# Kernel tuning notes

Hardware: AMD Instinct MI355X
Metric: run time of the kernel (lower is better)

Reference implementation:

```python
import jax, jax.numpy as jnp
import numpy as np

# Static configuration matching the selected code path:
#   mode='inject_subject', is_self_attn=True, layer_id='up_blocks.0' (inject layer, bank hit)
#   alpha = AlphaScheduler.alpha(step=20, total=50, 'up_blocks.0') = 0.8 * 0.6 = 0.48
B, L, D, H = 4, 1024, 1280, 20
DH = D // H  # 64
ALPHA = 0.48


def setup_inputs() -> dict:
    key = jax.random.key(0)
    ks = jax.random.split(key, 8)
    w = lambda k, shp: (jax.random.normal(k, shp, dtype=jnp.float32) * 0.02)
    return {
        "hidden_states": jax.random.normal(ks[0], (B, L, D), dtype=jnp.float32),
        "Wq": w(ks[1], (D, D)),
        "Wk": w(ks[2], (D, D)),
        "Wv": w(ks[3], (D, D)),
        "Wo": w(ks[4], (D, D)),
        "bo": jnp.zeros((D,), dtype=jnp.float32),
        # cached background K/V, stored after head_to_batch_dim -> [B*H, L_bg, DH]
        "K_bg": jax.random.normal(ks[5], (B * H, L, DH), dtype=jnp.float32),
        "V_bg": jax.random.normal(ks[6], (B * H, L, DH), dtype=jnp.float32),
    }


def _head_to_batch(x):  # [B, L, D] -> [B*H, L, DH]
    b, l, _ = x.shape
    return x.reshape(b, l, H, DH).transpose(0, 2, 1, 3).reshape(b * H, l, DH)


def _batch_to_head(x):  # [B*H, L, DH] -> [B, L, D]
    bh, l, _ = x.shape
    b = bh // H
    return x.reshape(b, H, l, DH).transpose(0, 2, 1, 3).reshape(b, l, D)


def reference(hidden_states, Wq, Wk, Wv, Wo, bo, K_bg, V_bg):
    # q/k/v projections (self-attention: k, v from hidden_states)
    q = _head_to_batch(hidden_states @ Wq)  # [B*H, L, DH]
    k = _head_to_batch(hidden_states @ Wk)
    v = _head_to_batch(hidden_states @ Wv)

    # inject_subject: concat cached background K/V scaled by alpha along kv-seq dim
    k = jnp.concatenate([k, ALPHA * K_bg], axis=1)  # [B*H, 2L, DH]
    v = jnp.concatenate([v, ALPHA * V_bg], axis=1)

    # _sdpa: q scaled by scale*sqrt(dh), SDPA divides by sqrt(dh) -> net factor `scale`
    scale = 1.0 / jnp.sqrt(jnp.asarray(DH, dtype=q.dtype))
    scores = jnp.einsum('bqd,bkd->bqk', q, k) * scale  # [B*H, L, 2L]
    probs = jax.nn.softmax(scores, axis=-1)
    context = jnp.einsum('bqk,bkd->bqd', probs, v)  # [B*H, L, DH]

    out = _batch_to_head(context) @ Wo + bo  # to_out[0] linear
    return out
```

## Files before the change

kernel.cpp:

```cpp
#include <hip/hip_runtime.h>
#include <hip/hip_bf16.h>

#define B_   4
#define L_   1024
#define D_   1280
#define H_   20
#define DH_  64
#define BH_  (B_*H_)
#define L2_  (2*L_)
#define ALPHA_ 0.48f
#define QSCALE_ 0.180336880f

typedef __attribute__((ext_vector_type(8))) short short8;
typedef __attribute__((ext_vector_type(4))) float float4v;

#define EXP2(x) exp2f(x)

__device__ __forceinline__ float bf2f(ushort u) {
    union { unsigned int i; float f; } v; v.i = ((unsigned int)u) << 16; return v.f;
}
__device__ __forceinline__ ushort f2bf(float f) {
    union { float f; unsigned int i; } v; v.f = f;
    unsigned int i = v.i;
    unsigned int r = i + 0x7FFF + ((i >> 16) & 1);
    return (ushort)(r >> 16);
}
__device__ __forceinline__ short8 pack8(float4 f0, float4 f1) {
    short8 o;
    o[0] = (short)f2bf(f0.x); o[1] = (short)f2bf(f0.y);
    o[2] = (short)f2bf(f0.z); o[3] = (short)f2bf(f0.w);
    o[4] = (short)f2bf(f1.x); o[5] = (short)f2bf(f1.y);
    o[6] = (short)f2bf(f1.z); o[7] = (short)f2bf(f1.w);
    return o;
}
__device__ __forceinline__ void pack4_store(ushort* dst, float a, float b, float c, float d) {
    union { __hip_bfloat162 h; unsigned int u; } x, y;
    x.h = __float22bfloat162_rn(make_float2(a, b));
    y.h = __float22bfloat162_rn(make_float2(c, d));
    uint2 v; v.x = x.u; v.y = y.u;
    *(uint2*)dst = v;
}

__device__ __forceinline__ void async16(const void* g, void* l) {
    __builtin_amdgcn_global_load_lds(
        (__attribute__((address_space(1))) void*)g,
        (__attribute__((address_space(3))) void*)l, 16, 0, 0);
}

__global__ __launch_bounds__(256) void detect_dtype(const unsigned int* __restrict__ w,
                                                    int* __restrict__ flag) {
    __shared__ int cnt;
    if (threadIdx.x == 0) cnt = 0;
    __syncthreads();
    int local = 0;
    for (int i = threadIdx.x; i < 4096; i += 256) {
        unsigned e = (w[i] >> 7) & 0xFF;
        local += (e >= 100 && e <= 130) ? 1 : 0;
    }
    atomicAdd(&cnt, local);
    __syncthreads();
    if (threadIdx.x == 0) flag[0] = (cnt > 2048) ? 1 : 0;
}

__global__ __launch_bounds__(256) void prep(
    const void* __restrict__ w0, const void* __restrict__ w1,
    const void* __restrict__ w2, const void* __restrict__ w3,
    ushort* __restrict__ Wt,
    const void* __restrict__ Vbg, ushort* __restrict__ Vt,
    const void* __restrict__ X, ushort* __restrict__ Xb,
    const void* __restrict__ Kbg, ushort* __restrict__ Kcv,
    const int* __restrict__ flag) {
    bool is16 = flag[0] != 0;
    int bi = blockIdx.x, tid = threadIdx.x;
    if (bi < 2880) {
        bool doScale = (bi >= 1600);
        const void* src; ushort* dst; int srcld, dstld; long sbase, dbase;
        if (bi < 1600) {
            int z = bi / 400, t4 = bi % 400;
            int by = t4 / 20, bx = t4 % 20;
            const void* srcs[4] = {w0, w1, w2, w3};
            src = srcs[z]; srcld = D_; dstld = D_;
            sbase = (long)(by * 64) * D_ + bx * 64;
            dst = Wt + (long)z * D_ * D_;
            dbase = (long)(bx * 64) * D_ + by * 64;
        } else {
            int j = bi - 1600;
            int bh = j >> 4, kt = j & 15;
            src = Vbg; srcld = DH_; dstld = L2_;
            sbase = ((long)bh * L_ + kt * 64) * DH_;
            dst = Vt;
            dbase = (long)bh * DH_ * L2_ + L_ + kt * 64;
        }
        __shared__ ushort t[64 * 72];
        int ldr = tid >> 3, ldc = (tid & 7) * 8;
#pragma unroll
        for (int i = 0; i < 2; i++) {
            int y = ldr + 32 * i;
            long idx = sbase + (long)y * srcld + ldc;
            short8 v;
            if (is16) {
                v = *(const short8*)((const ushort*)src + idx);
                if (doScale) {
#pragma unroll
                    for (int j2 = 0; j2 < 8; j2++)
                        v[j2] = (short)f2bf(ALPHA_ * bf2f((ushort)v[j2]));
                }
            } else {
                const float* s = (const float*)src;
                float4 f0 = *(const float4*)&s[idx];
                float4 f1 = *(const float4*)&s[idx + 4];
                if (doScale) {
                    f0.x *= ALPHA_; f0.y *= ALPHA_; f0.z *= ALPHA_; f0.w *= ALPHA_;
                    f1.x *= ALPHA_; f1.y *= ALPHA_; f1.z *= ALPHA_; f1.w *= ALPHA_;
                }
                v = pack8(f0, f1);
            }
            *(short8*)&t[y * 72 + ldc] = v;
        }
        __syncthreads();
        int c = tid & 63, r0 = (tid >> 6) * 16;
#pragma unroll
        for (int i = 0; i < 2; i++) {
            short8 o;
#pragma unroll
            for (int j2 = 0; j2 < 8; j2++) o[j2] = (short)t[(r0 + i * 8 + j2) * 72 + c];
            *(short8*)&dst[dbase + (long)c * dstld + r0 + i * 8] = o;
        }
    } else if (bi < 5440) {
        if (is16) return;
        long i = ((long)(bi - 2880) * 256 + tid) * 8;
        const float* s = (const float*)X;
        *(short8*)&Xb[i] = pack8(*(const float4*)&s[i], *(const float4*)&s[i + 4]);
    } else {
        if (is16) return;
        long i = ((long)(bi - 5440) * 256 + tid) * 8;
        const float* s = (const float*)Kbg;
        *(short8*)&Kcv[i] = pack8(*(const float4*)&s[i], *(const float4*)&s[i + 4]);
    }
}

template<int BMt, int BNt, int WROWS, int WCOLS>
__global__ __launch_bounds__(256) void gemm_tpl(
    const ushort* __restrict__ A16, const void* __restrict__ Araw,
    const ushort* __restrict__ Bt,
    ushort* __restrict__ Qp, ushort* __restrict__ Kp, ushort* __restrict__ Vt,
    void* __restrict__ Out, const void* __restrict__ bo, int mode,
    const int* __restrict__ flag) {
    constexpr int MI = BMt / WROWS / 16;
    constexpr int NI = BNt / WCOLS / 16;
    constexpr int ASZ = BMt * 32, BSZ = BNt * 32;
    constexpr int RB = 1280 / BNt;
    __shared__ __align__(16) ushort Al[2 * ASZ];
    __shared__ __align__(16) ushort Bl[2 * BSZ];
    bool is16 = flag[0] != 0;
    const ushort* A = (mode == 0 && is16) ? (const ushort*)Araw : A16;
    int tid = threadIdx.x;
    int bx = blockIdx.x, by = blockIdx.y;
    int w = tid >> 6, lane = tid & 63, l15 = lane & 15, quad = lane >> 4;
    int wm = (w / WCOLS) * (BMt / WROWS);
    int wn = (w % WCOLS) * (BNt / WCOLS);
    float4v acc[MI][NI] = {};
    const int K = 1280;
    constexpr int NK = 40;
    const ushort* Arow = A + (long)by * BMt * K + (tid >> 2) * K + (tid & 3) * 8;
    const ushort* Brow = Bt + (long)bx * BNt * K + (tid >> 2) * K + (tid & 3) * 8;

    auto stage = [&](int ki, int b) {
#pragma unroll
        for (int i = 0; i < BMt / 64; i++)
            async16(Arow + (long)i * 64 * K + ki * 32, &Al[b * ASZ + (i * 4 + w) * 512]);
#pragma unroll
        for (int i = 0; i < BNt / 64; i++)
            async16(Brow + (long)i * 64 * K + ki * 32, &Bl[b * BSZ + (i * 4 + w) * 512]);
    };

    stage(0, 0);
    __syncthreads();
    for (int ki = 0; ki < NK; ki++) {
        int cur = ki & 1;
        if (ki + 1 < NK) stage(ki + 1, 1 - cur);
        short8 av[MI], bv[NI];
#pragma unroll
        for (int mi = 0; mi < MI; mi++)
            av[mi] = *(const short8*)&Al[cur * ASZ + (wm + mi * 16 + l15) * 32 + quad * 8];
#pragma unroll
        for (int ni = 0; ni < NI; ni++)
            bv[ni] = *(const short8*)&Bl[cur * BSZ + (wn + ni * 16 + l15) * 32 + quad * 8];
#pragma unroll
        for (int mi = 0; mi < MI; mi++)
#pragma unroll
            for (int ni = 0; ni < NI; ni++)
                acc[mi][ni] = __builtin_amdgcn_mfma_f32_16x16x32_bf16(av[mi], bv[ni], acc[mi][ni], 0, 0, 0);
        __syncthreads();
    }

    if (mode == 0) {
        int which = bx / RB;
#pragma unroll
        for (int mi = 0; mi < MI; mi++) {
            int m0 = by * BMt + wm + mi * 16 + quad * 4;
            int b = m0 >> 10, l0 = m0 & 1023;
#pragma unroll
            for (int ni = 0; ni < NI; ni++) {
                int n = bx * BNt + wn + ni * 16 + l15;
                int np = n - which * 1280;
                int h = np >> 6, dh = np & 63;
                if (which == 0) {
#pragma unroll
                    for (int r = 0; r < 4; r++)
                        Qp[((long)(b * H_ + h) * L_ + l0 + r) * DH_ + dh] =
                            f2bf(acc[mi][ni][r] * QSCALE_);
                } else if (which == 1) {
#pragma unroll
                    for (int r = 0; r < 4; r++)
                        Kp[((long)(b * H_ + h) * L_ + l0 + r) * DH_ + dh] =
                            f2bf(acc[mi][ni][r]);
                } else {
                    pack4_store(&Vt[((long)(b * H_ + h) * DH_ + dh) * L2_ + l0],
                                acc[mi][ni][0], acc[mi][ni][1],
                                acc[mi][ni][2], acc[mi][ni][3]);
                }
            }
        }
    } else {
#pragma unroll
        for (int mi = 0; mi < MI; mi++) {
            int mloc = wm + mi * 16 + quad * 4;
#pragma unroll
            for (int ni = 0; ni < NI; ni++) {
                int nloc = wn + ni * 16 + l15;
#pragma unroll
                for (int r = 0; r < 4; r++) {
                    int m = by * BMt + mloc + r;
                    int n = bx * BNt + nloc;
                    float bias = is16 ? bf2f(((const ushort*)bo)[n]) : ((const float*)bo)[n];
                    float o = acc[mi][ni][r] + bias;
                    if (is16) ((ushort*)Out)[(long)m * D_ + n] = f2bf(o);
                    else      ((float*)Out)[(long)m * D_ + n] = o;
                }
            }
        }
    }
}

#define FS 72

__global__ __launch_bounds__(256) void flash_attn(
    const ushort* __restrict__ Qp, const ushort* __restrict__ Kp,
    const void* __restrict__ KbgRaw, const ushort* __restrict__ Kcv,
    const ushort* __restrict__ Vt, ushort* __restrict__ Ctx,
    const int* __restrict__ flag) {
    __shared__ __align__(16) ushort Kl[2 * 4096], Vl[2 * 4096];
    __shared__ __align__(16) ushort Pl[128 * FS];
    const ushort* Kbg = flag[0] ? (const ushort*)KbgRaw : Kcv;
    int tid = threadIdx.x;
    int w = tid >> 6, lane = tid & 63, l15 = lane & 15, quad = lane >> 4;
    int bi = blockIdx.x;
    int bh = (bi & 7) * 10 + ((bi >> 3) % 10);
    int qt = bi / 80;

    short8 aq[2][2];
    const ushort* Qb = Qp + ((long)bh * L_ + qt * 128 + w * 32) * DH_;
#pragma unroll
    for (int mi = 0; mi < 2; mi++)
#pragma unroll
        for (int ks = 0; ks < 2; ks++)
            aq[mi][ks] = *(const short8*)&Qb[(mi * 16 + l15) * DH_ + ks * 32 + quad * 8];

    float rs[2] = {0.f, 0.f};
    float4v O[2][4] = {};
    const ushort* Vb = Vt + (long)bh * DH_ * L2_;
    int prow = (w * 32 + l15) * FS;

    auto stage = [&](int kt, int b) {
        const ushort* Ksrc = (kt < 16)
            ? Kp  + ((long)bh * L_ + kt * 64) * DH_
            : Kbg + ((long)bh * L_ + (kt - 16) * 64) * DH_;
#pragma unroll
        for (int i = 0; i < 2; i++) {
            int q = i * 4 + w;
            async16(&Ksrc[(long)lane * DH_ + q * 8], &Kl[b * 4096 + q * 512]);
            async16(&Vb[(long)lane * L2_ + kt * 64 + q * 8], &Vl[b * 4096 + q * 512]);
        }
    };

    stage(0, 0);
    __syncthreads();
    for (int kt = 0; kt < 32; kt++) {
        int cur = kt & 1;
        if (kt + 1 < 32) stage(kt + 1, 1 - cur);
        bool bg = (kt >= 16);
        short8 bk[2][4];
#pragma unroll
        for (int ks = 0; ks < 2; ks++)
#pragma unroll
            for (int nt = 0; nt < 4; nt++)
                bk[ks][nt] = *(const short8*)&Kl[cur * 4096 + (ks * 4 + quad) * 512 + (nt * 16 + l15) * 8];
#pragma unroll
        for (int mi = 0; mi < 2; mi++) {
            float4v s[4] = {};
#pragma unroll
            for (int ks = 0; ks < 2; ks++)
#pragma unroll
                for (int nt = 0; nt < 4; nt++)
                    s[nt] = __builtin_amdgcn_mfma_f32_16x16x32_bf16(bk[ks][nt], aq[mi][ks], s[nt], 0, 0, 0);
#pragma unroll
            for (int nt = 0; nt < 4; nt++) {
                float p[4];
#pragma unroll
                for (int r = 0; r < 4; r++) {
                    float sv = s[nt][r];
                    if (bg) sv *= ALPHA_;
                    p[r] = EXP2(sv);
                    rs[mi] += p[r];
                }
                pack4_store(&Pl[prow + mi * 16 * FS + nt * 16 + quad * 4],
                            p[0], p[1], p[2], p[3]);
            }
        }
        short8 bv[2][4];
#pragma unroll
        for (int ks = 0; ks < 2; ks++)
#pragma unroll
            for (int nt = 0; nt < 4; nt++)
                bv[ks][nt] = *(const short8*)&Vl[cur * 4096 + (ks * 4 + quad) * 512 + (nt * 16 + l15) * 8];
        asm volatile("s_waitcnt lgkmcnt(0)" ::: "memory");
#pragma unroll
        for (int mi = 0; mi < 2; mi++)
#pragma unroll
            for (int ks = 0; ks < 2; ks++) {
                short8 ap = *(const short8*)&Pl[prow + mi * 16 * FS + ks * 32 + quad * 8];
#pragma unroll
                for (int nt = 0; nt < 4; nt++)
                    O[mi][nt] = __builtin_amdgcn_mfma_f32_16x16x32_bf16(bv[ks][nt], ap, O[mi][nt], 0, 0, 0);
            }
        __syncthreads();
    }
    float rcp[2];
#pragma unroll
    for (int mi = 0; mi < 2; mi++) {
        float v = rs[mi];
        v += __shfl_xor(v, 16);
        v += __shfl_xor(v, 32);
        rcp[mi] = 1.f / v;
    }
    int b = bh / H_, h = bh % H_;
#pragma unroll
    for (int mi = 0; mi < 2; mi++) {
        long l = qt * 128 + w * 32 + mi * 16 + l15;
#pragma unroll
        for (int nt = 0; nt < 4; nt++)
            pack4_store(&Ctx[(long)(b * L_ + l) * D_ + h * DH_ + nt * 16 + quad * 4],
                        O[mi][nt][0] * rcp[mi], O[mi][nt][1] * rcp[mi],
                        O[mi][nt][2] * rcp[mi], O[mi][nt][3] * rcp[mi]);
    }
}

extern "C" void kernel_launch(void* const* d_in, const int* in_sizes, int n_in,
                              void* d_out, int out_size, void* d_ws, size_t ws_size,
                              hipStream_t stream) {
    const void* X   = d_in[0];
    const void* Wq  = d_in[1];
    const void* Wk  = d_in[2];
    const void* Wv  = d_in[3];
    const void* Wo  = d_in[4];
    const void* bo  = d_in[5];
    const void* Kbg = d_in[6];
    const void* Vbg = d_in[7];

    char* ws = (char*)d_ws;
    size_t off = 0;
    auto alloc = [&](size_t bytes) {
        void* p = ws + off;
        off = (off + bytes + 255) & ~(size_t)255;
        return p;
    };
    int*    dflag = (int*)alloc(256);
    ushort* Wt    = (ushort*)alloc((size_t)4 * D_ * D_ * 2);
    ushort* Qp    = (ushort*)alloc((size_t)BH_ * L_ * DH_ * 2);
    ushort* Kp    = (ushort*)alloc((size_t)BH_ * L_ * DH_ * 2);
    ushort* Kcv   = (ushort*)alloc((size_t)BH_ * L_ * DH_ * 2);
    ushort* Vt    = (ushort*)alloc((size_t)BH_ * DH_ * L2_ * 2);
    ushort* Xb    = (ushort*)alloc((size_t)B_ * L_ * D_ * 2);
    ushort* Ctx   = Xb;
    ushort* Wqkv_t = Wt;
    ushort* Wo_t   = Wt + (size_t)3 * D_ * D_;

    dim3 tb(256);
    detect_dtype<<<1, tb, 0, stream>>>((const unsigned int*)Wq, dflag);
    prep<<<8000, tb, 0, stream>>>(Wq, Wk, Wv, Wo, Wt, Vbg, Vt, X, Xb, Kbg, Kcv, dflag);
    gemm_tpl<128, 64, 2, 2><<<dim3(60, 32), tb, 0, stream>>>(
        Xb, X, Wqkv_t, Qp, Kp, Vt, nullptr, nullptr, 0, dflag);
    flash_attn<<<dim3(640), tb, 0, stream>>>(Qp, Kp, Kbg, Kcv, Vt, Ctx, dflag);
    gemm_tpl<64, 64, 2, 2><<<dim3(20, 64), tb, 0, stream>>>(
        Ctx, nullptr, Wo_t, nullptr, nullptr, nullptr, d_out, bo, 1, dflag);
}
```

Before: 349.2 us.

## Software-pipeline PV MFMA one tile behind QK in flash attention, drop dtype detection

In the flash-attention loop, the P·V MFMA for the previous key tile now runs after the current tile's QK^T MFMAs. K and V staging is split so V for a tile is loaded one iteration later than K. This is meant to hide the exp/LDS-store latency and save one barrier per iteration. The change also swaps exp2f for a raw v_exp_f32 and removes the runtime dtype-detection kernel and its fp32/bf16 branches, so the code now assumes fp32 inputs.

```diff
diff --git a/kernel.cpp b/kernel.cpp
--- a/kernel.cpp
+++ b/kernel.cpp
@@ -14,11 +14,12 @@
 typedef __attribute__((ext_vector_type(8))) short short8;
 typedef __attribute__((ext_vector_type(4))) float float4v;
 
-#define EXP2(x) exp2f(x)
-
-__device__ __forceinline__ float bf2f(ushort u) {
-    union { unsigned int i; float f; } v; v.i = ((unsigned int)u) << 16; return v.f;
-}
+__device__ __forceinline__ float exp2_fast(float x) {
+    float r;
+    asm volatile("v_exp_f32 %0, %1" : "=v"(r) : "v"(x));
+    return r;
+}
+
 __device__ __forceinline__ ushort f2bf(float f) {
     union { float f; unsigned int i; } v; v.f = f;
     unsigned int i = v.i;
@@ -47,38 +48,21 @@
         (__attribute__((address_space(3))) void*)l, 16, 0, 0);
 }
 
-__global__ __launch_bounds__(256) void detect_dtype(const unsigned int* __restrict__ w,
-                                                    int* __restrict__ flag) {
-    __shared__ int cnt;
-    if (threadIdx.x == 0) cnt = 0;
-    __syncthreads();
-    int local = 0;
-    for (int i = threadIdx.x; i < 4096; i += 256) {
-        unsigned e = (w[i] >> 7) & 0xFF;
-        local += (e >= 100 && e <= 130) ? 1 : 0;
-    }
-    atomicAdd(&cnt, local);
-    __syncthreads();
-    if (threadIdx.x == 0) flag[0] = (cnt > 2048) ? 1 : 0;
-}
-
 __global__ __launch_bounds__(256) void prep(
-    const void* __restrict__ w0, const void* __restrict__ w1,
-    const void* __restrict__ w2, const void* __restrict__ w3,
+    const float* __restrict__ w0, const float* __restrict__ w1,
+    const float* __restrict__ w2, const float* __restrict__ w3,
     ushort* __restrict__ Wt,
-    const void* __restrict__ Vbg, ushort* __restrict__ Vt,
-    const void* __restrict__ X, ushort* __restrict__ Xb,
-    const void* __restrict__ Kbg, ushort* __restrict__ Kcv,
-    const int* __restrict__ flag) {
-    bool is16 = flag[0] != 0;
+    const float* __restrict__ Vbg, ushort* __restrict__ Vt,
+    const float* __restrict__ X, ushort* __restrict__ Xb,
+    const float* __restrict__ Kbg, ushort* __restrict__ Kcv) {
     int bi = blockIdx.x, tid = threadIdx.x;
     if (bi < 2880) {
         bool doScale = (bi >= 1600);
-        const void* src; ushort* dst; int srcld, dstld; long sbase, dbase;
+        const float* src; ushort* dst; int srcld, dstld; long sbase, dbase;
         if (bi < 1600) {
             int z = bi / 400, t4 = bi % 400;
             int by = t4 / 20, bx = t4 % 20;
-            const void* srcs[4] = {w0, w1, w2, w3};
+            const float* srcs[4] = {w0, w1, w2, w3};
             src = srcs[z]; srcld = D_; dstld = D_;
             sbase = (long)(by * 64) * D_ + bx * 64;
             dst = Wt + (long)z * D_ * D_;
@@ -97,25 +81,13 @@
         for (int i = 0; i < 2; i++) {
             int y = ldr + 32 * i;
             long idx = sbase + (long)y * srcld + ldc;
-            short8 v;
-            if (is16) {
-                v = *(const short8*)((const ushort*)src + idx);
-                if (doScale) {
-#pragma unroll
-                    for (int j2 = 0; j2 < 8; j2++)
-                        v[j2] = (short)f2bf(ALPHA_ * bf2f((ushort)v[j2]));
-                }
-            } else {
-                const float* s = (const float*)src;
-                float4 f0 = *(const float4*)&s[idx];
-                float4 f1 = *(const float4*)&s[idx + 4];
-                if (doScale) {
-                    f0.x *= ALPHA_; f0.y *= ALPHA_; f0.z *= ALPHA_; f0.w *= ALPHA_;
-                    f1.x *= ALPHA_; f1.y *= ALPHA_; f1.z *= ALPHA_; f1.w *= ALPHA_;
-                }
-                v = pack8(f0, f1);
-            }
-            *(short8*)&t[y * 72 + ldc] = v;
+            float4 f0 = *(const float4*)&src[idx];
+            float4 f1 = *(const float4*)&src[idx + 4];
+            if (doScale) {
+                f0.x *= ALPHA_; f0.y *= ALPHA_; f0.z *= ALPHA_; f0.w *= ALPHA_;
+                f1.x *= ALPHA_; f1.y *= ALPHA_; f1.z *= ALPHA_; f1.w *= ALPHA_;
+            }
+            *(short8*)&t[y * 72 + ldc] = pack8(f0, f1);
         }
         __syncthreads();
         int c = tid & 63, r0 = (tid >> 6) * 16;
@@ -127,33 +99,25 @@
             *(short8*)&dst[dbase + (long)c * dstld + r0 + i * 8] = o;
         }
     } else if (bi < 5440) {
-        if (is16) return;
         long i = ((long)(bi - 2880) * 256 + tid) * 8;
-        const float* s = (const float*)X;
-        *(short8*)&Xb[i] = pack8(*(const float4*)&s[i], *(const float4*)&s[i + 4]);
+        *(short8*)&Xb[i] = pack8(*(const float4*)&X[i], *(const float4*)&X[i + 4]);
     } else {
-        if (is16) return;
         long i = ((long)(bi - 5440) * 256 + tid) * 8;
-        const float* s = (const float*)Kbg;
-        *(short8*)&Kcv[i] = pack8(*(const float4*)&s[i], *(const float4*)&s[i + 4]);
+        *(short8*)&Kcv[i] = pack8(*(const float4*)&Kbg[i], *(const float4*)&Kbg[i + 4]);
     }
 }
 
 template<int BMt, int BNt, int WROWS, int WCOLS>
 __global__ __launch_bounds__(256) void gemm_tpl(
-    const ushort* __restrict__ A16, const void* __restrict__ Araw,
-    const ushort* __restrict__ Bt,
+    const ushort* __restrict__ A, const ushort* __restrict__ Bt,
     ushort* __restrict__ Qp, ushort* __restrict__ Kp, ushort* __restrict__ Vt,
-    void* __restrict__ Out, const void* __restrict__ bo, int mode,
-    const int* __restrict__ flag) {
+    float* __restrict__ Out, const float* __restrict__ bo, int mode) {
     constexpr int MI = BMt / WROWS / 16;
     constexpr int NI = BNt / WCOLS / 16;
     constexpr int ASZ = BMt * 32, BSZ = BNt * 32;
     constexpr int RB = 1280 / BNt;
     __shared__ __align__(16) ushort Al[2 * ASZ];
     __shared__ __align__(16) ushort Bl[2 * BSZ];
-    bool is16 = flag[0] != 0;
-    const ushort* A = (mode == 0 && is16) ? (const ushort*)Araw : A16;
     int tid = threadIdx.x;
     int bx = blockIdx.x, by = blockIdx.y;
     int w = tid >> 6, lane = tid & 63, l15 = lane & 15, quad = lane >> 4;
@@ -233,10 +197,7 @@
                 for (int r = 0; r < 4; r++) {
                     int m = by * BMt + mloc + r;
                     int n = bx * BNt + nloc;
-                    float bias = is16 ? bf2f(((const ushort*)bo)[n]) : ((const float*)bo)[n];
-                    float o = acc[mi][ni][r] + bias;
-                    if (is16) ((ushort*)Out)[(long)m * D_ + n] = f2bf(o);
-                    else      ((float*)Out)[(long)m * D_ + n] = o;
+                    Out[(long)m * D_ + n] = acc[mi][ni][r] + bo[n];
                 }
             }
         }
@@ -247,12 +208,10 @@
 
 __global__ __launch_bounds__(256) void flash_attn(
     const ushort* __restrict__ Qp, const ushort* __restrict__ Kp,
-    const void* __restrict__ KbgRaw, const ushort* __restrict__ Kcv,
-    const ushort* __restrict__ Vt, ushort* __restrict__ Ctx,
-    const int* __restrict__ flag) {
+    const ushort* __restrict__ Kbg, const ushort* __restrict__ Vt,
+    ushort* __restrict__ Ctx) {
     __shared__ __align__(16) ushort Kl[2 * 4096], Vl[2 * 4096];
     __shared__ __align__(16) ushort Pl[128 * FS];
-    const ushort* Kbg = flag[0] ? (const ushort*)KbgRaw : Kcv;
     int tid = threadIdx.x;
     int w = tid >> 6, lane = tid & 63, l15 = lane & 15, quad = lane >> 4;
     int bi = blockIdx.x;
@@ -272,58 +231,86 @@
     const ushort* Vb = Vt + (long)bh * DH_ * L2_;
     int prow = (w * 32 + l15) * FS;
 
-    auto stage = [&](int kt, int b) {
+    auto stageK = [&](int kt) {
         const ushort* Ksrc = (kt < 16)
             ? Kp  + ((long)bh * L_ + kt * 64) * DH_
             : Kbg + ((long)bh * L_ + (kt - 16) * 64) * DH_;
 #pragma unroll
         for (int i = 0; i < 2; i++) {
             int q = i * 4 + w;
-            async16(&Ksrc[(long)lane * DH_ + q * 8], &Kl[b * 4096 + q * 512]);
-            async16(&Vb[(long)lane * L2_ + kt * 64 + q * 8], &Vl[b * 4096 + q * 512]);
+            async16(&Ksrc[(long)lane * DH_ + q * 8], &Kl[(kt & 1) * 4096 + q * 512]);
         }
     };
-
-    stage(0, 0);
+    auto stageV = [&](int kt) {
+#pragma unroll
+        for (int i = 0; i < 2; i++) {
+            int q = i * 4 + w;
+            async16(&Vb[(long)lane * L2_ + kt * 64 + q * 8], &Vl[(kt & 1) * 4096 + q * 512]);
+        }
+    };
+
+    stageK(0);
     __syncthreads();
     for (int kt = 0; kt < 32; kt++) {
         int cur = kt & 1;
-        if (kt + 1 < 32) stage(kt + 1, 1 - cur);
-        bool bg = (kt >= 16);
+        if (kt + 1 < 32) stageK(kt + 1);
+        stageV(kt);
         short8 bk[2][4];
 #pragma unroll
         for (int ks = 0; ks < 2; ks++)
 #pragma unroll
             for (int nt = 0; nt < 4; nt++)
                 bk[ks][nt] = *(const short8*)&Kl[cur * 4096 + (ks * 4 + quad) * 512 + (nt * 16 + l15) * 8];
-#pragma unroll
-        for (int mi = 0; mi < 2; mi++) {
-            float4v s[4] = {};
+        float4v s[2][4] = {};
+#pragma unroll
+        for (int mi = 0; mi < 2; mi++)
 #pragma unroll
             for (int ks = 0; ks < 2; ks++)
 #pragma unroll
                 for (int nt = 0; nt < 4; nt++)
-                    s[nt] = __builtin_amdgcn_mfma_f32_16x16x32_bf16(bk[ks][nt], aq[mi][ks], s[nt], 0, 0, 0);
+                    s[mi][nt] = __builtin_amdgcn_mfma_f32_16x16x32_bf16(bk[ks][nt], aq[mi][ks], s[mi][nt], 0, 0, 0);
+        if (kt > 0) {
+            short8 bv[2][4];
+#pragma unroll
+            for (int ks = 0; ks < 2; ks++)
+#pragma unroll
+                for (int nt = 0; nt < 4; nt++)
+                    bv[ks][nt] = *(const short8*)&Vl[(1 - cur) * 4096 + (ks * 4 + quad) * 512 + (nt * 16 + l15) * 8];
+#pragma unroll
+            for (int mi = 0; mi < 2; mi++)
+#pragma unroll
+                for (int ks = 0; ks < 2; ks++) {
+                    short8 ap = *(const short8*)&Pl[prow + mi * 16 * FS + ks * 32 + quad * 8];
+#pragma unroll
+                    for (int nt = 0; nt < 4; nt++)
+                        O[mi][nt] = __builtin_amdgcn_mfma_f32_16x16x32_bf16(bv[ks][nt], ap, O[mi][nt], 0, 0, 0);
+                }
+        }
+        bool bg = (kt >= 16);
+#pragma unroll
+        for (int mi = 0; mi < 2; mi++)
 #pragma unroll
             for (int nt = 0; nt < 4; nt++) {
                 float p[4];
 #pragma unroll
                 for (int r = 0; r < 4; r++) {
-                    float sv = s[nt][r];
+                    float sv = s[mi][nt][r];
                     if (bg) sv *= ALPHA_;
-                    p[r] = EXP2(sv);
+                    p[r] = exp2_fast(sv);
                     rs[mi] += p[r];
                 }
                 pack4_store(&Pl[prow + mi * 16 * FS + nt * 16 + quad * 4],
                             p[0], p[1], p[2], p[3]);
             }
-        }
+        __syncthreads();
+    }
+    {
         short8 bv[2][4];
 #pragma unroll
         for (int ks = 0; ks < 2; ks++)
 #pragma unroll
             for (int nt = 0; nt < 4; nt++)
-                bv[ks][nt] = *(const short8*)&Vl[cur * 4096 + (ks * 4 + quad) * 512 + (nt * 16 + l15) * 8];
+                bv[ks][nt] = *(const short8*)&Vl[4096 + (ks * 4 + quad) * 512 + (nt * 16 + l15) * 8];
         asm volatile("s_waitcnt lgkmcnt(0)" ::: "memory");
 #pragma unroll
         for (int mi = 0; mi < 2; mi++)
@@ -334,7 +321,6 @@
                 for (int nt = 0; nt < 4; nt++)
                     O[mi][nt] = __builtin_amdgcn_mfma_f32_16x16x32_bf16(bv[ks][nt], ap, O[mi][nt], 0, 0, 0);
             }
-        __syncthreads();
     }
     float rcp[2];
 #pragma unroll
@@ -359,14 +345,14 @@
 extern "C" void kernel_launch(void* const* d_in, const int* in_sizes, int n_in,
                               void* d_out, int out_size, void* d_ws, size_t ws_size,
                               hipStream_t stream) {
-    const void* X   = d_in[0];
-    const void* Wq  = d_in[1];
-    const void* Wk  = d_in[2];
-    const void* Wv  = d_in[3];
-    const void* Wo  = d_in[4];
-    const void* bo  = d_in[5];
-    const void* Kbg = d_in[6];
-    const void* Vbg = d_in[7];
+    const float* X   = (const float*)d_in[0];
+    const float* Wq  = (const float*)d_in[1];
+    const float* Wk  = (const float*)d_in[2];
+    const float* Wv  = (const float*)d_in[3];
+    const float* Wo  = (const float*)d_in[4];
+    const float* bo  = (const float*)d_in[5];
+    const float* Kbg = (const float*)d_in[6];
+    const float* Vbg = (const float*)d_in[7];
 
     char* ws = (char*)d_ws;
     size_t off = 0;
@@ -375,7 +361,6 @@
         off = (off + bytes + 255) & ~(size_t)255;
         return p;
     };
-    int*    dflag = (int*)alloc(256);
     ushort* Wt    = (ushort*)alloc((size_t)4 * D_ * D_ * 2);
     ushort* Qp    = (ushort*)alloc((size_t)BH_ * L_ * DH_ * 2);
     ushort* Kp    = (ushort*)alloc((size_t)BH_ * L_ * DH_ * 2);
@@ -387,11 +372,10 @@
     ushort* Wo_t   = Wt + (size_t)3 * D_ * D_;
 
     dim3 tb(256);
-    detect_dtype<<<1, tb, 0, stream>>>((const unsigned int*)Wq, dflag);
-    prep<<<8000, tb, 0, stream>>>(Wq, Wk, Wv, Wo, Wt, Vbg, Vt, X, Xb, Kbg, Kcv, dflag);
+    prep<<<8000, tb, 0, stream>>>(Wq, Wk, Wv, Wo, Wt, Vbg, Vt, X, Xb, Kbg, Kcv);
     gemm_tpl<128, 64, 2, 2><<<dim3(60, 32), tb, 0, stream>>>(
-        Xb, X, Wqkv_t, Qp, Kp, Vt, nullptr, nullptr, 0, dflag);
-    flash_attn<<<dim3(640), tb, 0, stream>>>(Qp, Kp, Kbg, Kcv, Vt, Ctx, dflag);
+        Xb, Wqkv_t, Qp, Kp, Vt, nullptr, nullptr, 0);
+    flash_attn<<<dim3(640), tb, 0, stream>>>(Qp, Kp, Kcv, Vt, Ctx);
     gemm_tpl<64, 64, 2, 2><<<dim3(20, 64), tb, 0, stream>>>(
-        Ctx, nullptr, Wo_t, nullptr, nullptr, nullptr, d_out, bo, 1, dflag);
-}
+        Ctx, Wo_t, nullptr, nullptr, nullptr, (float*)d_out, bo, 1);
+}
```

After: 370.5 us. 6.1% more time.
